# Kernel optimization log

Measured on AMD Instinct MI355X. Metric: run time of the kernel, lower is better.

Reference implementation:

```python
import jax, jax.numpy as jnp
import numpy as np

TEMPERATURE = 0.1

def setup_inputs() -> dict:
    key = jax.random.key(0)
    k1, k2 = jax.random.split(key)
    A = jax.random.normal(k1, (16, 2048, 256), dtype=jnp.float32)
    B = jax.random.normal(k2, (16, 2048, 256), dtype=jnp.float32)
    return {"A": A, "B": B}

def _l2norm(x):
    # F.normalize(p=2, dim=-1): x / max(||x||, eps), eps=1e-12
    n = jnp.sqrt(jnp.sum(x * x, axis=-1, keepdims=True))
    return x / jnp.maximum(n, 1e-12)

def _nce_dir(sim):
    # sim: (B, N, N) logits; labels are the diagonal (row n -> col n)
    # mean over all B*N rows of (logsumexp(row) - row[label])
    lse = jax.nn.logsumexp(sim, axis=-1)            # (B, N)
    diag = jnp.diagonal(sim, axis1=-2, axis2=-1)    # (B, N)
    return jnp.mean(lse - diag)

def reference(A, B):
    emb1 = _l2norm(A)
    emb2 = _l2norm(B)
    sim12 = jnp.einsum("bnc,bmc->bnm", emb1, emb2) / TEMPERATURE  # (B, N, N)
    # sim21 is sim12 transposed per batch; reuse instead of a second bmm
    sim21 = jnp.swapaxes(sim12, -1, -2)
    return _nce_dir(sim12) + _nce_dir(sim21)
```

## Files before the change

kernel.cpp:

```cpp
#include <hip/hip_runtime.h>
#include <hip/hip_bf16.h>

typedef __attribute__((ext_vector_type(8))) __bf16 bf16x8;
typedef __attribute__((ext_vector_type(16))) float f32x16;

#define SCALE_L2E 14.4269504088896f
#define NTOT 32768

#define AS_GLOBAL __attribute__((address_space(1)))
#define AS_LDS    __attribute__((address_space(3)))

__device__ inline void async_copy16(const void* g, void* l) {
    __builtin_amdgcn_global_load_lds((const AS_GLOBAL void*)g, (AS_LDS void*)l, 16, 0, 0);
}

__device__ inline unsigned int f2bf(float f) {
    unsigned int u = __builtin_bit_cast(unsigned int, f);
    u += 0x7fffu + ((u >> 16) & 1u);
    return u >> 16;
}

__device__ inline uint4 pack8(float4 x, float4 y, float s) {
    uint4 r;
    r.x = f2bf(x.x * s) | (f2bf(x.y * s) << 16);
    r.y = f2bf(x.z * s) | (f2bf(x.w * s) << 16);
    r.z = f2bf(y.x * s) | (f2bf(y.y * s) << 16);
    r.w = f2bf(y.z * s) | (f2bf(y.w * s) << 16);
    return r;
}

__device__ inline float dot8(float4 x, float4 y) {
    return x.x*y.x + x.y*y.y + x.z*y.z + x.w*y.w;
}

__global__ __launch_bounds__(256) void nrm_kernel(
        const float* __restrict__ A, const float* __restrict__ B,
        uint4* __restrict__ E1f, uint4* __restrict__ E2f,
        float* __restrict__ diagPart, float* __restrict__ scalars,
        unsigned int* __restrict__ counter) {
    const int tid = threadIdx.x, w = tid >> 6, l = tid & 63;
    const int q = l & 31, h = l >> 5;
    const int wid = blockIdx.x * 4 + w;

    const float4* A4 = (const float4*)A + ((size_t)wid * 8 + h) * 64 + q * 2;
    const float4* B4 = (const float4*)B + ((size_t)wid * 8 + h) * 64 + q * 2;

    float4 a[8], bb[8];
    #pragma unroll
    for (int i = 0; i < 4; ++i) {
        a[2*i]    = A4[i * 128];
        a[2*i+1]  = A4[i * 128 + 1];
        bb[2*i]   = B4[i * 128];
        bb[2*i+1] = B4[i * 128 + 1];
    }

    float ddAcc = 0.f;
    #pragma unroll
    for (int i = 0; i < 4; ++i) {
        float sa = dot8(a[2*i], a[2*i]) + dot8(a[2*i+1], a[2*i+1]);
        float sb = dot8(bb[2*i], bb[2*i]) + dot8(bb[2*i+1], bb[2*i+1]);
        float dd = dot8(a[2*i], bb[2*i]) + dot8(a[2*i+1], bb[2*i+1]);
        #pragma unroll
        for (int off = 1; off <= 16; off <<= 1) {
            sa += __shfl_xor(sa, off);
            sb += __shfl_xor(sb, off);
            dd += __shfl_xor(dd, off);
        }
        const float ia = 1.0f / fmaxf(sqrtf(sa), 1e-12f);
        const float ib = 1.0f / fmaxf(sqrtf(sb), 1e-12f);
        if (q == 0) ddAcc += dd * ia * ib * 10.0f;

        const int n0 = wid * 8 + i * 2 + h;
        const size_t chunk = (size_t)(n0 >> 11) * 65536
                           + (size_t)((n0 & 2047) >> 5) * 1024
                           + (q >> 1) * 64 + (q & 1) * 32 + (n0 & 31);
        E1f[chunk] = pack8(a[2*i], a[2*i+1], ia * SCALE_L2E);
        E2f[chunk] = pack8(bb[2*i], bb[2*i+1], ib);
    }

    #pragma unroll
    for (int off = 1; off <= 32; off <<= 1) ddAcc += __shfl_xor(ddAcc, off);
    __shared__ float part[4];
    if (l == 0) part[w] = ddAcc;
    __syncthreads();
    if (tid == 0) diagPart[blockIdx.x] = part[0] + part[1] + part[2] + part[3];
    if (blockIdx.x == 0 && tid == 0) { scalars[0] = 0.f; *counter = 0u; }
}

__global__ __launch_bounds__(256, 2) void gemm_kernel(
        const bf16x8* __restrict__ E1f, const uint4* __restrict__ E2f,
        float* __restrict__ colPart, float* __restrict__ rowPart) {
    __shared__ bf16x8 Bbuf[2][2048];
    __shared__ float colLDS[2048];

    const int tid = threadIdx.x, w = tid >> 6, l = tid & 63;
    const int b = blockIdx.x & 15;
    const int ct = (blockIdx.x >> 4) & 3, rt = blockIdx.x >> 6;

    for (int i = l; i < 512; i += 64) colLDS[w * 512 + i] = 0.f;

    const uint4* Bb = E2f + (size_t)b * 65536 + (size_t)ct * 16384 + l;

    auto stage = [&](int buf, int sg) {
        const uint4* src = Bb + (size_t)sg * 2048 + (w * 8) * 64;
        #pragma unroll
        for (int j = 0; j < 8; ++j)
            async_copy16(src + j * 64, &Bbuf[buf][(w * 8 + j) * 64]);
    };

    stage(0, 0);

    const bf16x8* Af0 = E1f + (size_t)b * 65536 + (size_t)(rt * 8 + w * 2) * 1024 + l;
    const bf16x8* Af1 = Af0 + 1024;
    bf16x8 af0[16], af1[16];
    #pragma unroll
    for (int kt = 0; kt < 16; ++kt) { af0[kt] = Af0[kt * 64]; af1[kt] = Af1[kt * 64]; }

    float rowAcc0[16], rowAcc1[16];
    #pragma unroll
    for (int r = 0; r < 16; ++r) { rowAcc0[r] = 0.f; rowAcc1[r] = 0.f; }

    __syncthreads();

    for (int sg = 0; sg < 8; ++sg) {
        if (sg < 7) stage((sg + 1) & 1, sg + 1);

        const bf16x8* Bf = Bbuf[sg & 1];
        for (int half = 0; half < 2; ++half) {
            f32x16 acc0, acc1;
            #pragma unroll
            for (int r = 0; r < 16; ++r) { acc0[r] = 0.f; acc1[r] = 0.f; }

            #pragma unroll
            for (int kt = 0; kt < 16; ++kt) {
                bf16x8 bfrag = Bf[half * 1024 + kt * 64 + l];
                acc0 = __builtin_amdgcn_mfma_f32_32x32x16_bf16(af0[kt], bfrag, acc0, 0, 0, 0);
                acc1 = __builtin_amdgcn_mfma_f32_32x32x16_bf16(af1[kt], bfrag, acc1, 0, 0, 0);
            }

            float p = 0.f;
            #pragma unroll
            for (int r = 0; r < 16; ++r) {
                float e0 = exp2f(acc0[r] - SCALE_L2E);
                float e1 = exp2f(acc1[r] - SCALE_L2E);
                rowAcc0[r] += e0;
                rowAcc1[r] += e1;
                p += e0 + e1;
            }
            p += __shfl_xor(p, 32);
            if (l < 32) colLDS[w * 512 + (sg * 2 + half) * 32 + l] += p;
        }
        __syncthreads();
    }

    #pragma unroll
    for (int r = 0; r < 16; ++r) {
        #pragma unroll
        for (int off = 1; off <= 16; off <<= 1) {
            rowAcc0[r] += __shfl_xor(rowAcc0[r], off);
            rowAcc1[r] += __shfl_xor(rowAcc1[r], off);
        }
    }
    if ((l & 31) == 0) {
        float* rs = rowPart + (size_t)(b * 4 + ct) * 2048 + rt * 256 + w * 64 + 4 * (l >> 5);
        #pragma unroll
        for (int r = 0; r < 16; ++r) {
            const int rl = (r & 3) + 8 * (r >> 2);
            rs[rl]      = rowAcc0[r];
            rs[rl + 32] = rowAcc1[r];
        }
    }

    __syncthreads();
    float* gcol = colPart + (size_t)((b * 4 + ct) * 8 + rt) * 512;
    for (int i = tid; i < 512; i += 256)
        gcol[i] = colLDS[i] + colLDS[512 + i] + colLDS[1024 + i] + colLDS[1536 + i];
}

__global__ __launch_bounds__(256) void fin_kernel(
        const float* __restrict__ colPart, const float* __restrict__ rowPart,
        const float* __restrict__ diagPart, float* __restrict__ scalars,
        unsigned int* __restrict__ counter, float* __restrict__ out) {
    const int tid = threadIdx.x;
    float s = 0.f;
    #pragma unroll
    for (int k = 0; k < 2; ++k) {
        const int g = blockIdx.x * 512 + k * 256 + tid;
        const float* cp = colPart + (size_t)(((g >> 11) * 4 + ((g >> 9) & 3)) * 8) * 512 + (g & 511);
        float cs = 0.f;
        #pragma unroll
        for (int rt = 0; rt < 8; ++rt) cs += cp[rt * 512];
        const float* rp = rowPart + (size_t)(g >> 11) * 4 * 2048 + (g & 2047);
        float rsum = rp[0] + rp[2048] + rp[4096] + rp[6144];
        s += logf(cs) + logf(rsum);
    }
    #pragma unroll
    for (int off = 1; off <= 32; off <<= 1) s += __shfl_xor(s, off);
    __shared__ float part[4];
    __shared__ unsigned int lastFlag;
    if ((tid & 63) == 0) part[tid >> 6] = s;
    __syncthreads();
    if (tid == 0) {
        atomicAdd(&scalars[0], part[0] + part[1] + part[2] + part[3]);
        __threadfence();
        lastFlag = (atomicAdd(counter, 1u) == 63u) ? 1u : 0u;
    }
    __syncthreads();
    if (lastFlag) {
        float d = diagPart[tid] + diagPart[tid + 256]
                + diagPart[tid + 512] + diagPart[tid + 768];
        #pragma unroll
        for (int off = 1; off <= 32; off <<= 1) d += __shfl_xor(d, off);
        if ((tid & 63) == 0) part[tid >> 6] = d;
        __syncthreads();
        if (tid == 0) {
            const float diag = part[0] + part[1] + part[2] + part[3];
            const float logSum = atomicAdd(&scalars[0], 0.f);
            out[0] = (logSum - 2.0f * diag) / (float)NTOT + 20.0f;
        }
    }
}

extern "C" void kernel_launch(void* const* d_in, const int* in_sizes, int n_in,
                              void* d_out, int out_size, void* d_ws, size_t ws_size,
                              hipStream_t stream) {
    const float* A = (const float*)d_in[0];
    const float* B = (const float*)d_in[1];

    char* w = (char*)d_ws;
    uint4* E1f = (uint4*)w;
    uint4* E2f = (uint4*)(w + (size_t)16 * 1024 * 1024);
    float* colPart = (float*)(w + (size_t)32 * 1024 * 1024);
    float* rowPart = colPart + 262144;
    float* diagPart = rowPart + 131072;
    float* scalars = diagPart + 1024;
    unsigned int* counter = (unsigned int*)(scalars + 1);

    hipLaunchKernelGGL(nrm_kernel, dim3(1024), dim3(256), 0, stream,
                       A, B, E1f, E2f, diagPart, scalars, counter);
    hipLaunchKernelGGL(gemm_kernel, dim3(512), dim3(256), 0, stream,
                       (const bf16x8*)E1f, (const uint4*)E2f, colPart, rowPart);
    hipLaunchKernelGGL(fin_kernel, dim3(64), dim3(256), 0, stream,
                       colPart, rowPart, diagPart, scalars, counter, (float*)d_out);
}
```

Before: 157.2 us.

## Fuse finalize reduction into GEMM via atomic tile counters, halve norm work per wave

Drops the separate finalize kernel. Each GEMM block bumps per-column-tile and per-row-tile atomic counters, and the last block to finish a tile computes the log-sums and adds them into a global scalar. A final global counter lets the last block write the output. The norm kernel now launches twice as many blocks, each doing half the rows, with nontemporal loads. The GEMM folds the -SCALE bias into the accumulator init and uses hardware exp2/log builtins. This removes one kernel launch and spreads the tail reduction across blocks, at the cost of extra atomics and fences in every GEMM block.

```diff
diff --git a/kernel.cpp b/kernel.cpp
--- a/kernel.cpp
+++ b/kernel.cpp
@@ -3,6 +3,7 @@
 
 typedef __attribute__((ext_vector_type(8))) __bf16 bf16x8;
 typedef __attribute__((ext_vector_type(16))) float f32x16;
+typedef __attribute__((ext_vector_type(4))) float f32x4;
 
 #define SCALE_L2E 14.4269504088896f
 #define NTOT 32768
@@ -12,6 +13,22 @@
 
 __device__ inline void async_copy16(const void* g, void* l) {
     __builtin_amdgcn_global_load_lds((const AS_GLOBAL void*)g, (AS_LDS void*)l, 16, 0, 0);
+}
+
+__device__ inline float fast_exp2(float x) {
+#if __has_builtin(__builtin_amdgcn_exp2f)
+    return __builtin_amdgcn_exp2f(x);
+#else
+    return exp2f(x);
+#endif
+}
+
+__device__ inline float fast_ln(float x) {
+#if __has_builtin(__builtin_amdgcn_logf)
+    return __builtin_amdgcn_logf(x) * 0.6931471805599453f;
+#else
+    return logf(x);
+#endif
 }
 
 __device__ inline unsigned int f2bf(float f) {
@@ -20,7 +37,7 @@
     return u >> 16;
 }
 
-__device__ inline uint4 pack8(float4 x, float4 y, float s) {
+__device__ inline uint4 pack8(f32x4 x, f32x4 y, float s) {
     uint4 r;
     r.x = f2bf(x.x * s) | (f2bf(x.y * s) << 16);
     r.y = f2bf(x.z * s) | (f2bf(x.w * s) << 16);
@@ -29,7 +46,7 @@
     return r;
 }
 
-__device__ inline float dot8(float4 x, float4 y) {
+__device__ inline float dot8(f32x4 x, f32x4 y) {
     return x.x*y.x + x.y*y.y + x.z*y.z + x.w*y.w;
 }
 
@@ -37,26 +54,31 @@
         const float* __restrict__ A, const float* __restrict__ B,
         uint4* __restrict__ E1f, uint4* __restrict__ E2f,
         float* __restrict__ diagPart, float* __restrict__ scalars,
-        unsigned int* __restrict__ counter) {
+        unsigned int* __restrict__ ctr) {
     const int tid = threadIdx.x, w = tid >> 6, l = tid & 63;
     const int q = l & 31, h = l >> 5;
     const int wid = blockIdx.x * 4 + w;
 
-    const float4* A4 = (const float4*)A + ((size_t)wid * 8 + h) * 64 + q * 2;
-    const float4* B4 = (const float4*)B + ((size_t)wid * 8 + h) * 64 + q * 2;
-
-    float4 a[8], bb[8];
-    #pragma unroll
-    for (int i = 0; i < 4; ++i) {
-        a[2*i]    = A4[i * 128];
-        a[2*i+1]  = A4[i * 128 + 1];
-        bb[2*i]   = B4[i * 128];
-        bb[2*i+1] = B4[i * 128 + 1];
+    if (blockIdx.x == 0) {
+        if (tid < 224) ctr[tid] = 0u;
+        if (tid == 0) scalars[0] = 0.f;
+    }
+
+    const f32x4* A4 = (const f32x4*)A + ((size_t)wid * 4 + h) * 64 + q * 2;
+    const f32x4* B4 = (const f32x4*)B + ((size_t)wid * 4 + h) * 64 + q * 2;
+
+    f32x4 a[4], bb[4];
+    #pragma unroll
+    for (int i = 0; i < 2; ++i) {
+        a[2*i]    = __builtin_nontemporal_load(A4 + i * 128);
+        a[2*i+1]  = __builtin_nontemporal_load(A4 + i * 128 + 1);
+        bb[2*i]   = __builtin_nontemporal_load(B4 + i * 128);
+        bb[2*i+1] = __builtin_nontemporal_load(B4 + i * 128 + 1);
     }
 
     float ddAcc = 0.f;
     #pragma unroll
-    for (int i = 0; i < 4; ++i) {
+    for (int i = 0; i < 2; ++i) {
         float sa = dot8(a[2*i], a[2*i]) + dot8(a[2*i+1], a[2*i+1]);
         float sb = dot8(bb[2*i], bb[2*i]) + dot8(bb[2*i+1], bb[2*i+1]);
         float dd = dot8(a[2*i], bb[2*i]) + dot8(a[2*i+1], bb[2*i+1]);
@@ -70,7 +92,7 @@
         const float ib = 1.0f / fmaxf(sqrtf(sb), 1e-12f);
         if (q == 0) ddAcc += dd * ia * ib * 10.0f;
 
-        const int n0 = wid * 8 + i * 2 + h;
+        const int n0 = wid * 4 + i * 2 + h;
         const size_t chunk = (size_t)(n0 >> 11) * 65536
                            + (size_t)((n0 & 2047) >> 5) * 1024
                            + (q >> 1) * 64 + (q & 1) * 32 + (n0 & 31);
@@ -84,12 +106,13 @@
     if (l == 0) part[w] = ddAcc;
     __syncthreads();
     if (tid == 0) diagPart[blockIdx.x] = part[0] + part[1] + part[2] + part[3];
-    if (blockIdx.x == 0 && tid == 0) { scalars[0] = 0.f; *counter = 0u; }
 }
 
 __global__ __launch_bounds__(256, 2) void gemm_kernel(
         const bf16x8* __restrict__ E1f, const uint4* __restrict__ E2f,
-        float* __restrict__ colPart, float* __restrict__ rowPart) {
+        float* __restrict__ colPart, float* __restrict__ rowPart,
+        const float* __restrict__ diagPart, float* __restrict__ scalars,
+        unsigned int* __restrict__ ctr, float* __restrict__ out) {
     __shared__ bf16x8 Bbuf[2][2048];
     __shared__ float colLDS[2048];
 
@@ -129,7 +152,9 @@
         for (int half = 0; half < 2; ++half) {
             f32x16 acc0, acc1;
             #pragma unroll
-            for (int r = 0; r < 16; ++r) { acc0[r] = 0.f; acc1[r] = 0.f; }
+            for (int r = 0; r < 16; ++r) {
+                acc0[r] = -SCALE_L2E; acc1[r] = -SCALE_L2E;
+            }
 
             #pragma unroll
             for (int kt = 0; kt < 16; ++kt) {
@@ -141,8 +166,8 @@
             float p = 0.f;
             #pragma unroll
             for (int r = 0; r < 16; ++r) {
-                float e0 = exp2f(acc0[r] - SCALE_L2E);
-                float e1 = exp2f(acc1[r] - SCALE_L2E);
+                float e0 = fast_exp2(acc0[r]);
+                float e1 = fast_exp2(acc1[r]);
                 rowAcc0[r] += e0;
                 rowAcc1[r] += e1;
                 p += e0 + e1;
@@ -175,46 +200,61 @@
     float* gcol = colPart + (size_t)((b * 4 + ct) * 8 + rt) * 512;
     for (int i = tid; i < 512; i += 256)
         gcol[i] = colLDS[i] + colLDS[512 + i] + colLDS[1024 + i] + colLDS[1536 + i];
-}
-
-__global__ __launch_bounds__(256) void fin_kernel(
-        const float* __restrict__ colPart, const float* __restrict__ rowPart,
-        const float* __restrict__ diagPart, float* __restrict__ scalars,
-        unsigned int* __restrict__ counter, float* __restrict__ out) {
-    const int tid = threadIdx.x;
-    float s = 0.f;
-    #pragma unroll
-    for (int k = 0; k < 2; ++k) {
-        const int g = blockIdx.x * 512 + k * 256 + tid;
-        const float* cp = colPart + (size_t)(((g >> 11) * 4 + ((g >> 9) & 3)) * 8) * 512 + (g & 511);
-        float cs = 0.f;
-        #pragma unroll
-        for (int rt = 0; rt < 8; ++rt) cs += cp[rt * 512];
-        const float* rp = rowPart + (size_t)(g >> 11) * 4 * 2048 + (g & 2047);
-        float rsum = rp[0] + rp[2048] + rp[4096] + rp[6144];
-        s += logf(cs) + logf(rsum);
-    }
-    #pragma unroll
-    for (int off = 1; off <= 32; off <<= 1) s += __shfl_xor(s, off);
-    __shared__ float part[4];
-    __shared__ unsigned int lastFlag;
-    if ((tid & 63) == 0) part[tid >> 6] = s;
-    __syncthreads();
+
+    __threadfence();
+    __shared__ int flags;
     if (tid == 0) {
-        atomicAdd(&scalars[0], part[0] + part[1] + part[2] + part[3]);
-        __threadfence();
-        lastFlag = (atomicAdd(counter, 1u) == 63u) ? 1u : 0u;
-    }
-    __syncthreads();
-    if (lastFlag) {
-        float d = diagPart[tid] + diagPart[tid + 256]
-                + diagPart[tid + 512] + diagPart[tid + 768];
+        int f = 0;
+        if (atomicAdd(&ctr[16 + (b * 4 + ct)], 1u) == 7u) f |= 1;
+        if (atomicAdd(&ctr[96 + (b * 8 + rt)], 1u) == 3u) f |= 2;
+        flags = f;
+    }
+    __syncthreads();
+    const int f = flags;
+    if (f) {
+        float myLog = 0.f;
+        if (f & 1) {
+            const float* cp = colPart + (size_t)(b * 4 + ct) * 8 * 512;
+            #pragma unroll
+            for (int k = 0; k < 2; ++k) {
+                const int c = k * 256 + tid;
+                float cs = 0.f;
+                #pragma unroll
+                for (int j = 0; j < 8; ++j) cs += cp[j * 512 + c];
+                myLog += fast_ln(cs);
+            }
+        }
+        if (f & 2) {
+            const float* rp = rowPart + rt * 256 + tid;
+            float rsv = 0.f;
+            #pragma unroll
+            for (int j = 0; j < 4; ++j) rsv += rp[(size_t)(b * 4 + j) * 2048];
+            myLog += fast_ln(rsv);
+        }
+        #pragma unroll
+        for (int off = 1; off <= 32; off <<= 1) myLog += __shfl_xor(myLog, off);
+        __shared__ float lpart[4];
+        if (l == 0) lpart[w] = myLog;
+        __syncthreads();
+        if (tid == 0)
+            atomicAdd(&scalars[0], lpart[0] + lpart[1] + lpart[2] + lpart[3]);
+    }
+
+    __threadfence();
+    __shared__ int lastF;
+    if (tid == 0) lastF = (atomicAdd(&ctr[0], 1u) == 511u) ? 1 : 0;
+    __syncthreads();
+    if (lastF) {
+        float d = 0.f;
+        #pragma unroll
+        for (int j = 0; j < 8; ++j) d += diagPart[j * 256 + tid];
         #pragma unroll
         for (int off = 1; off <= 32; off <<= 1) d += __shfl_xor(d, off);
-        if ((tid & 63) == 0) part[tid >> 6] = d;
+        __shared__ float dpart[4];
+        if (l == 0) dpart[w] = d;
         __syncthreads();
         if (tid == 0) {
-            const float diag = part[0] + part[1] + part[2] + part[3];
+            const float diag = dpart[0] + dpart[1] + dpart[2] + dpart[3];
             const float logSum = atomicAdd(&scalars[0], 0.f);
             out[0] = (logSum - 2.0f * diag) / (float)NTOT + 20.0f;
         }
@@ -233,13 +273,12 @@
     float* colPart = (float*)(w + (size_t)32 * 1024 * 1024);
     float* rowPart = colPart + 262144;
     float* diagPart = rowPart + 131072;
-    float* scalars = diagPart + 1024;
-    unsigned int* counter = (unsigned int*)(scalars + 1);
-
-    hipLaunchKernelGGL(nrm_kernel, dim3(1024), dim3(256), 0, stream,
-                       A, B, E1f, E2f, diagPart, scalars, counter);
+    float* scalars = diagPart + 2048;
+    unsigned int* ctr = (unsigned int*)(scalars + 2);
+
+    hipLaunchKernelGGL(nrm_kernel, dim3(2048), dim3(256), 0, stream,
+                       A, B, E1f, E2f, diagPart, scalars, ctr);
     hipLaunchKernelGGL(gemm_kernel, dim3(512), dim3(256), 0, stream,
-                       (const bf16x8*)E1f, (const uint4*)E2f, colPart, rowPart);
-    hipLaunchKernelGGL(fin_kernel, dim3(64), dim3(256), 0, stream,
-                       colPart, rowPart, diagPart, scalars, counter, (float*)d_out);
-}
+                       (const bf16x8*)E1f, (const uint4*)E2f, colPart, rowPart,
+                       diagPart, scalars, ctr, (float*)d_out);
+}
```

After: 219.9 us. 39.9% more time.
